# Kernel tuning notes

Hardware: AMD Instinct MI355X
Metric: run time of the kernel (lower is better)

## Reference

```python
import jax, jax.numpy as jnp
import numpy as np

D_INPUT = 900; D_MODEL = 900; D_STATE = 16; D_CONV = 4
D_INNER = 1800; DT_RANK = 57  # ceil(900/16)
B_SZ = 2; L = 900


def build_pe():
    # Faithful to the (non-standard) loop in PositionalEncoding.__init__
    pos = np.arange(D_INPUT, dtype=np.float64)[:, None]
    pe = np.zeros((D_INPUT, D_MODEL), dtype=np.float64)
    i_even = np.arange(0, D_MODEL, 2, dtype=np.float64)
    i_odd = np.arange(1, D_MODEL, 2, dtype=np.float64)
    pe[:, 0::2] = np.sin(pos / 10000.0 ** (2.0 * i_even / D_MODEL))
    pe[:, 1::2] = np.cos(pos / 10000.0 ** (2.0 * (i_odd + 1.0) / D_MODEL))
    return jnp.asarray(pe, jnp.float32)


def setup_inputs() -> dict:
    key = jax.random.key(0)
    ks = jax.random.split(key, 8)
    s = 0.02
    inp = jax.random.normal(ks[0], (B_SZ, L, D_INPUT), jnp.float32)
    W_emb = jax.random.normal(ks[1], (D_MODEL, D_INPUT), jnp.float32) * s
    b_emb = jnp.zeros((D_MODEL,), jnp.float32)
    norm_w = jnp.ones((D_MODEL,), jnp.float32)
    W_in = jax.random.normal(ks[2], (2 * D_INNER, D_MODEL), jnp.float32) * s
    conv_w = jax.random.normal(ks[3], (D_INNER, 1, D_CONV), jnp.float32) * s
    conv_b = jnp.zeros((D_INNER,), jnp.float32)
    W_xp = jax.random.normal(ks[4], (DT_RANK + 2 * D_STATE, D_INNER), jnp.float32) * s
    W_dt = jax.random.normal(ks[5], (D_INNER, DT_RANK), jnp.float32) * s
    b_dt = jnp.zeros((D_INNER,), jnp.float32)
    A_log = jnp.log(jnp.broadcast_to(jnp.arange(1, D_STATE + 1, dtype=jnp.float32), (D_INNER, D_STATE)))
    D = jnp.ones((D_INNER,), jnp.float32)
    W_out = jax.random.normal(ks[6], (D_MODEL, D_INNER), jnp.float32) * s
    normf_w = jnp.ones((D_MODEL,), jnp.float32)
    pe = build_pe()
    return dict(inp=inp, W_emb=W_emb, b_emb=b_emb, norm_w=norm_w, W_in=W_in,
                conv_w=conv_w, conv_b=conv_b, W_xp=W_xp, W_dt=W_dt, b_dt=b_dt,
                A_log=A_log, D=D, W_out=W_out, normf_w=normf_w, pe=pe)


def rmsnorm(x, w, eps=1e-5):
    return x * jax.lax.rsqrt(jnp.mean(x * x, axis=-1, keepdims=True) + eps) * w


def causal_dwconv(x, w, b):
    # x: (b, l, d_in); torch Conv1d(groups=d_in, padding=k-1) then [:, :, :l] == causal left-pad
    xc = jnp.transpose(x, (0, 2, 1))  # (b, d_in, l)
    y = jax.lax.conv_general_dilated(xc, w, window_strides=(1,),
                                     padding=[(D_CONV - 1, 0)],
                                     dimension_numbers=('NCH', 'OIH', 'NCH'),
                                     feature_group_count=D_INNER)
    return jnp.transpose(y + b[None, :, None], (0, 2, 1))


def selective_scan(u, delta, A, Bm, Cm, Dv):
    # u, delta: (b, l, d_in); A: (d_in, n); Bm, Cm: (b, l, n); Dv: (d_in,)
    dA = jnp.exp(jnp.einsum('bld,dn->bldn', delta, A))
    dBu = jnp.einsum('bld,bln,bld->bldn', delta, Bm, u)

    def step(h, xs):
        dA_i, dBu_i, C_i = xs
        h = dA_i * h + dBu_i                      # (b, d_in, n)
        y = jnp.einsum('bdn,bn->bd', h, C_i)
        return h, y

    h0 = jnp.zeros((u.shape[0], D_INNER, D_STATE), u.dtype)
    _, ys = jax.lax.scan(step, h0, (jnp.moveaxis(dA, 1, 0), jnp.moveaxis(dBu, 1, 0), jnp.moveaxis(Cm, 1, 0)))
    return jnp.moveaxis(ys, 0, 1) + u * Dv


def mamba_block(x, W_in, conv_w, conv_b, W_xp, W_dt, b_dt, A_log, Dv, W_out):
    xr = x @ W_in.T                               # (b, l, 2*d_inner)
    xm, res = xr[..., :D_INNER], xr[..., D_INNER:]
    xb = xm[..., ::-1]  # NOTE: original flips dim 2 == channel dim, not sequence
    xm = jax.nn.silu(causal_dwconv(xm, conv_w, conv_b))
    xb = jax.nn.silu(causal_dwconv(xb, conv_w, conv_b))

    def ssm(u):
        A = -jnp.exp(A_log)
        xd = u @ W_xp.T                           # (b, l, dt_rank + 2n)
        delta = jax.nn.softplus(xd[..., :DT_RANK] @ W_dt.T + b_dt)
        Bm = xd[..., DT_RANK:DT_RANK + D_STATE]
        Cm = xd[..., DT_RANK + D_STATE:]
        return selective_scan(u, delta, A, Bm, Cm, Dv)

    y = ssm(xm)
    yb = ssm(xb)[..., ::-1]  # flip back over channels, as in original
    g = jax.nn.silu(res)
    return (y * g + yb * g) @ W_out.T


def reference(inp, W_emb, b_emb, norm_w, W_in, conv_w, conv_b, W_xp, W_dt, b_dt, A_log, D, W_out, normf_w, pe):
    x = inp @ W_emb.T + b_emb                     # embedding Linear
    x = x * jnp.sqrt(jnp.float32(D_MODEL)) + pe[None, :x.shape[1]]
    x = mamba_block(rmsnorm(x, norm_w), W_in, conv_w, conv_b, W_xp, W_dt, b_dt, A_log, D, W_out) + x
    x = rmsnorm(x, normf_w)
    logits = x.reshape(x.shape[0], -1)
    return (logits,)
```

## Files before the change

### kernel.cpp

```cpp
#include <hip/hip_runtime.h>
#include <math.h>

typedef unsigned short ushortT;
typedef short short8 __attribute__((ext_vector_type(8)));
typedef float f32x4 __attribute__((ext_vector_type(4)));

#define D_STATE 16
#define D_INNER 1800
#define DT_RANK 57
#define SEQ_L 900
#define MROWS 1800
#define MP 1920
#define KP_DM 960
#define KP_DI 1856
#define KP_DT 64
#define NCHUNK 45
#define CLEN 20

__device__ __forceinline__ ushortT f2bf(float f) {
    unsigned u = __float_as_uint(f);
    unsigned r = (u + 0x7FFFu + ((u >> 16) & 1u)) >> 16;
    return (ushortT)r;
}
__device__ __forceinline__ float bf2f(ushortT h) {
    return __uint_as_float((unsigned)h << 16);
}
__device__ __forceinline__ float silu_f(float x) { return x / (1.f + __expf(-x)); }
__device__ __forceinline__ float softplus_f(float x) {
    return fmaxf(x, 0.f) + __logf(1.f + __expf(-fabsf(x)));
}

__device__ __forceinline__ void gload_lds16(const ushortT* g, ushortT* l) {
    __builtin_amdgcn_global_load_lds((const __attribute__((address_space(1))) unsigned int*)g,
                                     (__attribute__((address_space(3))) unsigned int*)l,
                                     16, 0, 0);
}

__global__ __launch_bounds__(256)
void cvt_all_k(const float* __restrict__ s0, ushortT* __restrict__ d0,
               const float* __restrict__ s1, ushortT* __restrict__ d1,
               const float* __restrict__ s2, ushortT* __restrict__ d2,
               const float* __restrict__ s3, ushortT* __restrict__ d3,
               const float* __restrict__ s4, ushortT* __restrict__ d4,
               const float* __restrict__ s5, ushortT* __restrict__ d5)
{
    const float* src; ushortT* dst; int M, K, Mp, Kp;
    switch (blockIdx.y) {
      case 0: src=s0; dst=d0; M=1800; K=900;  Mp=1920; Kp=960;  break;
      case 1: src=s1; dst=d1; M=900;  K=900;  Mp=1024; Kp=960;  break;
      case 2: src=s2; dst=d2; M=3600; K=900;  Mp=3712; Kp=960;  break;
      case 3: src=s3; dst=d3; M=89;   K=1800; Mp=128;  Kp=1856; break;
      case 4: src=s4; dst=d4; M=1800; K=57;   Mp=1920; Kp=64;   break;
      default:src=s5; dst=d5; M=900;  K=1800; Mp=1024; Kp=1856; break;
    }
    int t = blockIdx.x * 256 + threadIdx.x;
    int K4 = Kp >> 2;
    if (t >= Mp * K4) return;
    int r = t / K4, c4 = (t - r * K4) * 4;
    ushortT o[4];
#pragma unroll
    for (int e = 0; e < 4; ++e) {
        int c = c4 + e;
        float v = (r < M && c < K) ? src[(size_t)r * K + c] : 0.f;
        o[e] = f2bf(v);
    }
    uint2 pk;
    pk.x = (unsigned)o[0] | ((unsigned)o[1] << 16);
    pk.y = (unsigned)o[2] | ((unsigned)o[3] << 16);
    *(uint2*)(dst + (size_t)r * Kp + c4) = pk;
}

__global__ __launch_bounds__(256)
void gemm_mfma_k(const ushortT* __restrict__ A0, const ushortT* __restrict__ A1, int lda,
                 const ushortT* __restrict__ Bw, int ldb, int nkTotal, int split,
                 float* __restrict__ C0, float* __restrict__ C1, int ldc, size_t cstride,
                 ushortT* __restrict__ X0, ushortT* __restrict__ X1, int ldx, size_t xstride,
                 int M, int N, const float* __restrict__ bias, int mode)
{
    __shared__ ushortT As[128 * 64];
    __shared__ ushortT Bs[128 * 64];
    int z = blockIdx.z;
    int dir = z / split, s = z % split;
    int per = (nkTotal + split - 1) / split;
    int kt0 = s * per;
    int kcnt = nkTotal - kt0; if (kcnt > per) kcnt = per;

    const ushortT* A = dir ? A1 : A0;
    float* C = (dir ? C1 : C0);
    ushortT* Xo = (dir ? X1 : X0);
    if (C)  C  += (size_t)s * cstride;
    if (Xo) Xo += (size_t)s * xstride;

    int tid = threadIdx.x;
    int lane = tid & 63, wave = tid >> 6;
    int wr = wave >> 1, wc = wave & 1;
    int m0 = blockIdx.y * 128, n0 = blockIdx.x * 128;

    f32x4 acc[4][4] = {};

    for (int kt = kt0; kt < kt0 + kcnt; ++kt) {
#pragma unroll
        for (int r = 0; r < 4; ++r) {
            int idx = r * 256 + tid;
            int row = idx >> 3, c8 = (idx & 7) << 3;
            gload_lds16(A + (size_t)(m0 + row) * lda + kt * 64 + c8, As + idx * 8);
        }
#pragma unroll
        for (int r = 0; r < 4; ++r) {
            int idx = r * 256 + tid;
            int row = idx >> 3, c8 = (idx & 7) << 3;
            gload_lds16(Bw + (size_t)(n0 + row) * ldb + kt * 64 + c8, Bs + idx * 8);
        }
        __syncthreads();
#pragma unroll
        for (int ks = 0; ks < 2; ++ks) {
            short8 av[4], bv[4];
            int kcol = ks * 32 + (lane >> 4) * 8;
#pragma unroll
            for (int i = 0; i < 4; ++i)
                av[i] = *(const short8*)(As + (wr * 64 + i * 16 + (lane & 15)) * 64 + kcol);
#pragma unroll
            for (int j = 0; j < 4; ++j)
                bv[j] = *(const short8*)(Bs + (wc * 64 + j * 16 + (lane & 15)) * 64 + kcol);
#pragma unroll
            for (int i = 0; i < 4; ++i)
#pragma unroll
                for (int j = 0; j < 4; ++j)
                    acc[i][j] = __builtin_amdgcn_mfma_f32_16x16x32_bf16(bv[j], av[i], acc[i][j], 0, 0, 0);
        }
        __syncthreads();
    }

#pragma unroll
    for (int i = 0; i < 4; ++i) {
        int m = m0 + wr * 64 + i * 16 + (lane & 15);
        if (m >= M) continue;
#pragma unroll
        for (int j = 0; j < 4; ++j) {
            int nb = n0 + wc * 64 + j * 16 + (lane >> 4) * 4;
            if (nb >= N) continue;
            f32x4 v = acc[i][j];
            if (mode == 5) {
#pragma unroll
                for (int e = 0; e < 4; ++e)
                    v[e] = softplus_f(v[e] + bias[nb + e]);
            }
            if (mode == 1 || mode == 5) {
                unsigned lo, hi;
                asm("v_cvt_pk_bf16_f32 %0, %1, %2" : "=v"(lo) : "v"(v[0]), "v"(v[1]));
                asm("v_cvt_pk_bf16_f32 %0, %1, %2" : "=v"(hi) : "v"(v[2]), "v"(v[3]));
                uint2 pk; pk.x = lo; pk.y = hi;
                *(uint2*)(Xo + (size_t)m * ldx + nb) = pk;
            } else {
                *(f32x4*)(C + (size_t)m * ldc + nb) = v;
            }
        }
    }
}

__global__ __launch_bounds__(256)
void rmsnorm_emb_k(const ushortT* __restrict__ P, size_t pstride,
                   const float* __restrict__ b_emb, const float* __restrict__ pe,
                   const float* __restrict__ norm_w,
                   float* __restrict__ XS, ushortT* __restrict__ XN, int ldxn)
{
    int row = blockIdx.x;
    int l = (row >= SEQ_L) ? row - SEQ_L : row;
    float vv[4];
    float ssum = 0.f;
#pragma unroll
    for (int k = 0; k < 4; ++k) {
        int c = threadIdx.x + k * 256;
        if (c < 900) {
            size_t i = (size_t)row * 900 + c;
            float a = bf2f(P[i]) + bf2f(P[i + pstride]) + bf2f(P[i + 2 * pstride]) + bf2f(P[i + 3 * pstride]);
            float v = 30.f * (a + b_emb[c]) + pe[(size_t)l * 900 + c];
            vv[k] = v;
            ssum += v * v;
        } else vv[k] = 0.f;
    }
#pragma unroll
    for (int off = 32; off; off >>= 1) ssum += __shfl_down(ssum, off, 64);
    __shared__ float red[4];
    int wv = threadIdx.x >> 6;
    if ((threadIdx.x & 63) == 0) red[wv] = ssum;
    __syncthreads();
    float tot = red[0] + red[1] + red[2] + red[3];
    float scale = rsqrtf(tot / 900.f + 1e-5f);
#pragma unroll
    for (int k = 0; k < 4; ++k) {
        int c = threadIdx.x + k * 256;
        if (c < 900) {
            XS[(size_t)row * 900 + c] = vv[k];
            XN[(size_t)row * ldxn + c] = f2bf(vv[k] * scale * norm_w[c]);
        }
    }
}

__global__ __launch_bounds__(256)
void rmsnorm_final_k(const ushortT* __restrict__ ZP, size_t zstride,
                     const float* __restrict__ XS, const float* __restrict__ w,
                     float* __restrict__ out)
{
    int row = blockIdx.x;
    float vv[4];
    float ssum = 0.f;
#pragma unroll
    for (int k = 0; k < 4; ++k) {
        int c = threadIdx.x + k * 256;
        if (c < 900) {
            size_t i = (size_t)row * 900 + c;
            float v = bf2f(ZP[i]) + bf2f(ZP[i + zstride]) + bf2f(ZP[i + 2 * zstride]) + bf2f(ZP[i + 3 * zstride]) + XS[i];
            vv[k] = v;
            ssum += v * v;
        } else vv[k] = 0.f;
    }
#pragma unroll
    for (int off = 32; off; off >>= 1) ssum += __shfl_down(ssum, off, 64);
    __shared__ float red[4];
    int wv = threadIdx.x >> 6;
    if ((threadIdx.x & 63) == 0) red[wv] = ssum;
    __syncthreads();
    float tot = red[0] + red[1] + red[2] + red[3];
    float scale = rsqrtf(tot / 900.f + 1e-5f);
#pragma unroll
    for (int k = 0; k < 4; ++k) {
        int c = threadIdx.x + k * 256;
        if (c < 900) out[(size_t)row * 900 + c] = vv[k] * scale * w[c];
    }
}

__global__ __launch_bounds__(256)
void conv_silu_k(const ushortT* __restrict__ xr0, const ushortT* __restrict__ xr1,
                 const float* __restrict__ w, const float* __restrict__ cb,
                 ushortT* __restrict__ xmc, ushortT* __restrict__ xbc,
                 ushortT* __restrict__ gout)
{
    int t = blockIdx.x * 256 + threadIdx.x;
    if (t >= MROWS * (D_INNER / 2)) return;
    int d0 = (t % (D_INNER / 2)) * 2;
    int row = t / (D_INNER / 2);
    int l = row % SEQ_L;
    float w0[4], w1[4];
#pragma unroll
    for (int k = 0; k < 4; ++k) { w0[k] = w[d0 * 4 + k]; w1[k] = w[d0 * 4 + 4 + k]; }
    int rdp = 1798 - d0;
    float sf0 = cb[d0], sf1 = cb[d0 + 1];
    float sb0 = sf0, sb1 = sf1;
#pragma unroll
    for (int k = 0; k < 4; ++k) {
        int ll = l - 3 + k;
        if (ll < 0) continue;
        size_t ro = (size_t)(row - l + ll) * 3600;
        unsigned f0 = *(const unsigned*)(xr0 + ro + d0);
        unsigned f1 = *(const unsigned*)(xr1 + ro + d0);
        float a0 = bf2f((ushortT)f0) + bf2f((ushortT)f1);
        float a1 = bf2f((ushortT)(f0 >> 16)) + bf2f((ushortT)(f1 >> 16));
        sf0 = fmaf(w0[k], a0, sf0);
        sf1 = fmaf(w1[k], a1, sf1);
        unsigned r0 = *(const unsigned*)(xr0 + ro + rdp);
        unsigned r1 = *(const unsigned*)(xr1 + ro + rdp);
        float b0 = bf2f((ushortT)(r0 >> 16)) + bf2f((ushortT)(r1 >> 16));
        float b1 = bf2f((ushortT)r0) + bf2f((ushortT)r1);
        sb0 = fmaf(w0[k], b0, sb0);
        sb1 = fmaf(w1[k], b1, sb1);
    }
    unsigned om = (unsigned)f2bf(silu_f(sf0)) | ((unsigned)f2bf(silu_f(sf1)) << 16);
    unsigned ob = (unsigned)f2bf(silu_f(sb0)) | ((unsigned)f2bf(silu_f(sb1)) << 16);
    *(unsigned*)(xmc + (size_t)row * KP_DI + d0) = om;
    *(unsigned*)(xbc + (size_t)row * KP_DI + d0) = ob;
    size_t rr = (size_t)row * 3600 + D_INNER + d0;
    unsigned g0 = *(const unsigned*)(xr0 + rr);
    unsigned g1 = *(const unsigned*)(xr1 + rr);
    float ga = silu_f(bf2f((ushortT)g0) + bf2f((ushortT)g1));
    float gb = silu_f(bf2f((ushortT)(g0 >> 16)) + bf2f((ushortT)(g1 >> 16)));
    *(unsigned*)(gout + (size_t)row * D_INNER + d0) = (unsigned)f2bf(ga) | ((unsigned)f2bf(gb) << 16);
}

__global__ __launch_bounds__(256)
void xp_reduce_k(const float* __restrict__ XPp, size_t pstride,
                 float* __restrict__ XDC, ushortT* __restrict__ XDMb, ushortT* __restrict__ XDBb)
{
    int t = blockIdx.x * 256 + threadIdx.x;
    if (t >= 2 * MROWS * 96) return;
    int dir = t / (MROWS * 96);
    int rem = t - dir * (MROWS * 96);
    int row = rem / 96, c = rem - row * 96;
    const float* basep = XPp + (size_t)dir * 8 * pstride + (size_t)row * 96 + c;
    float s = 0.f;
#pragma unroll
    for (int p = 0; p < 8; ++p) s += basep[p * pstride];
    ushortT* xdb = dir ? XDBb : XDMb;
    if (c < DT_RANK)           xdb[(size_t)row * KP_DT + c] = f2bf(s);
    else if (c < KP_DT)        xdb[(size_t)row * KP_DT + c] = 0;
    if (c >= DT_RANK && c < DT_RANK + 2 * D_STATE)
        XDC[((size_t)dir * MROWS + row) * 32 + (c - DT_RANK)] = s;
}

__global__ __launch_bounds__(256)
void scan_l1_k(const ushortT* __restrict__ DMb, const ushortT* __restrict__ DBb,
               const ushortT* __restrict__ Um, const ushortT* __restrict__ Ub,
               const float* __restrict__ XDC, const float* __restrict__ A_log,
               float* __restrict__ HL, float* __restrict__ SD)
{
    int d = blockIdx.x * 256 + threadIdx.x;
    if (d >= D_INNER) return;
    int c = blockIdx.y, zz = blockIdx.z;
    int b = zz >> 1, dir = zz & 1;
    const ushortT* DL = dir ? DBb : DMb;
    const ushortT* U = dir ? Ub : Um;
    const float* XD = XDC + (size_t)dir * MROWS * 32;
    float Aa[D_STATE];
#pragma unroll
    for (int n = 0; n < D_STATE; ++n) Aa[n] = -__expf(A_log[d * D_STATE + n]);
    float h[D_STATE] = {};
    float S = 0.f;
    int l0 = c * CLEN;
    for (int i = 0; i < CLEN; ++i) {
        size_t rowi = (size_t)b * SEQ_L + l0 + i;
        float delta = bf2f(DL[rowi * D_INNER + d]);
        float u = bf2f(U[rowi * KP_DI + d]);
        const float* bc = XD + rowi * 32;
        float du = delta * u;
        S += delta;
#pragma unroll
        for (int n = 0; n < D_STATE; ++n)
            h[n] = fmaf(__expf(delta * Aa[n]), h[n], du * bc[n]);
    }
    float* hp = HL + ((size_t)(zz * NCHUNK + c) * D_INNER + d) * D_STATE;
#pragma unroll
    for (int q = 0; q < 4; ++q)
        *(f32x4*)(hp + q * 4) = f32x4{h[q*4], h[q*4+1], h[q*4+2], h[q*4+3]};
    SD[(size_t)(zz * NCHUNK + c) * D_INNER + d] = S;
}

__global__ __launch_bounds__(256)
void scan_l2_k(float* __restrict__ HL, const float* __restrict__ SD,
               const float* __restrict__ A_log)
{
    int t = blockIdx.x * 256 + threadIdx.x;
    if (t >= 4 * D_INNER * D_STATE) return;
    int n = t & 15;
    int d = (t >> 4) % D_INNER;
    int zz = t / (D_INNER * D_STATE);
    float Aa = -__expf(A_log[d * D_STATE + n]);
    float h0 = 0.f;
    for (int c = 0; c < NCHUNK; ++c) {
        size_t ih = ((size_t)(zz * NCHUNK + c) * D_INNER + d) * D_STATE + n;
        float hl = HL[ih];
        float T = __expf(Aa * SD[(size_t)(zz * NCHUNK + c) * D_INNER + d]);
        HL[ih] = h0;
        h0 = fmaf(T, h0, hl);
    }
}

__global__ __launch_bounds__(256)
void scan3_gate_k(const ushortT* __restrict__ DMb, const ushortT* __restrict__ DBb,
                  const ushortT* __restrict__ Um, const ushortT* __restrict__ Ub,
                  const float* __restrict__ XDC, const float* __restrict__ A_log,
                  const float* __restrict__ Dv, const float* __restrict__ HL,
                  const ushortT* __restrict__ G, ushortT* __restrict__ YC)
{
    int d = blockIdx.x * 256 + threadIdx.x;
    if (d >= D_INNER) return;
    int c = blockIdx.y, b = blockIdx.z;
    int rd = D_INNER - 1 - d;
    float Aa0[D_STATE], Aa1[D_STATE], h0[D_STATE], h1[D_STATE];
#pragma unroll
    for (int n = 0; n < D_STATE; ++n) Aa0[n] = -__expf(A_log[d * D_STATE + n]);
#pragma unroll
    for (int n = 0; n < D_STATE; ++n) Aa1[n] = -__expf(A_log[rd * D_STATE + n]);
    const float* hp0 = HL + ((size_t)((b * 2) * NCHUNK + c) * D_INNER + d) * D_STATE;
    const float* hp1 = HL + ((size_t)((b * 2 + 1) * NCHUNK + c) * D_INNER + rd) * D_STATE;
#pragma unroll
    for (int q = 0; q < 4; ++q) {
        f32x4 t0 = *(const f32x4*)(hp0 + q * 4);
        f32x4 t1 = *(const f32x4*)(hp1 + q * 4);
        h0[q*4] = t0[0]; h0[q*4+1] = t0[1]; h0[q*4+2] = t0[2]; h0[q*4+3] = t0[3];
        h1[q*4] = t1[0]; h1[q*4+1] = t1[1]; h1[q*4+2] = t1[2]; h1[q*4+3] = t1[3];
    }
    float Dd0 = Dv[d], Dd1 = Dv[rd];
    const float* XD0 = XDC;
    const float* XD1 = XDC + (size_t)MROWS * 32;
    int l0 = c * CLEN;
    for (int i = 0; i < CLEN; ++i) {
        size_t rowi = (size_t)b * SEQ_L + l0 + i;
        float delta0 = bf2f(DMb[rowi * D_INNER + d]);
        float u0 = bf2f(Um[rowi * KP_DI + d]);
        const float* bc0 = XD0 + rowi * 32;
        float du0 = delta0 * u0;
        float acc0 = u0 * Dd0;
#pragma unroll
        for (int n = 0; n < D_STATE; ++n) {
            h0[n] = fmaf(__expf(delta0 * Aa0[n]), h0[n], du0 * bc0[n]);
            acc0 = fmaf(h0[n], bc0[D_STATE + n], acc0);
        }
        float delta1 = bf2f(DBb[rowi * D_INNER + rd]);
        float u1 = bf2f(Ub[rowi * KP_DI + rd]);
        const float* bc1 = XD1 + rowi * 32;
        float du1 = delta1 * u1;
        float acc1 = u1 * Dd1;
#pragma unroll
        for (int n = 0; n < D_STATE; ++n) {
            h1[n] = fmaf(__expf(delta1 * Aa1[n]), h1[n], du1 * bc1[n]);
            acc1 = fmaf(h1[n], bc1[D_STATE + n], acc1);
        }
        float g = bf2f(G[rowi * D_INNER + d]);
        YC[rowi * KP_DI + d] = f2bf((acc0 + acc1) * g);
    }
}

extern "C" void kernel_launch(void* const* d_in, const int* in_sizes, int n_in,
                              void* d_out, int out_size, void* d_ws, size_t ws_size,
                              hipStream_t stream)
{
    const float* inp    = (const float*)d_in[0];
    const float* W_emb  = (const float*)d_in[1];
    const float* b_emb  = (const float*)d_in[2];
    const float* norm_w = (const float*)d_in[3];
    const float* W_in   = (const float*)d_in[4];
    const float* conv_w = (const float*)d_in[5];
    const float* conv_b = (const float*)d_in[6];
    const float* W_xp   = (const float*)d_in[7];
    const float* W_dt   = (const float*)d_in[8];
    const float* b_dt   = (const float*)d_in[9];
    const float* A_log  = (const float*)d_in[10];
    const float* Dv     = (const float*)d_in[11];
    const float* W_out  = (const float*)d_in[12];
    const float* normf_w= (const float*)d_in[13];
    const float* pe     = (const float*)d_in[14];

    char* base = (char*)d_ws;
    size_t off = 0;
    auto alloc = [&](size_t bytes) { char* p = base + off; off += (bytes + 255) & ~(size_t)255; return p; };

    float*   XS      = (float*)alloc(6480000);
    char*    arena1  = alloc(22032000);
    float*   XPp     = (float*)arena1;
    float*   HL      = (float*)arena1;
    float*   SD      = (float*)(arena1 + 20736000);
    ushortT* inp_bf  = (ushortT*)alloc(3686400);
    ushortT* XN_bf   = (ushortT*)alloc(3686400);
    ushortT* Wemb_bf = (ushortT*)alloc(1966080);
    ushortT* Win_bf  = (ushortT*)alloc(7127040);
    ushortT* Wxp_bf  = (ushortT*)alloc(475136);
    ushortT* Wdt_bf  = (ushortT*)alloc(245760);
    ushortT* Wout_bf = (ushortT*)alloc(3801088);
    ushortT* XBC_bf  = (ushortT*)alloc(7127040);
    char*    arena2  = alloc(25920000);
    ushortT* Pemb    = (ushortT*)arena2;
    ushortT* XR0     = (ushortT*)arena2;
    ushortT* XR1     = XR0 + (size_t)MROWS * 3600;
    ushortT* DMb     = (ushortT*)arena2;
    ushortT* DBb     = DMb + (size_t)MROWS * D_INNER;
    ushortT* ZP      = (ushortT*)arena2;
    ushortT* G_bf    = (ushortT*)alloc(6480000);

    float*   XDC     = (float*)Wemb_bf;
    ushortT* XDM_bf  = (ushortT*)((char*)Wemb_bf + 460800);
    ushortT* XDB_bf  = (ushortT*)((char*)Wemb_bf + 706560);
    ushortT* XMC_bf  = Win_bf;
    ushortT* YC_bf   = inp_bf;

    dim3 blk(256);
    auto cdiv = [](int a, int b) { return (a + b - 1) / b; };
    const size_t PSTR  = 1620000;
    const size_t XPSTR = 172800;
    const size_t XRSTR = (size_t)MROWS * 3600;

    hipLaunchKernelGGL(cvt_all_k, dim3(3480, 6), blk, 0, stream,
                       inp, inp_bf, W_emb, Wemb_bf, W_in, Win_bf,
                       W_xp, Wxp_bf, W_dt, Wdt_bf, W_out, Wout_bf);
    hipLaunchKernelGGL(gemm_mfma_k, dim3(8, 15, 4), blk, 0, stream,
                       inp_bf, inp_bf, KP_DM, Wemb_bf, KP_DM, KP_DM/64, 4,
                       (float*)nullptr, (float*)nullptr, 0, (size_t)0,
                       Pemb, Pemb, 900, PSTR,
                       MROWS, 900, (const float*)nullptr, 1);
    hipLaunchKernelGGL(rmsnorm_emb_k, dim3(MROWS), blk, 0, stream,
                       Pemb, PSTR, b_emb, pe, norm_w, XS, XN_bf, KP_DM);
    hipLaunchKernelGGL(gemm_mfma_k, dim3(29, 15, 2), blk, 0, stream,
                       XN_bf, XN_bf, KP_DM, Win_bf, KP_DM, KP_DM/64, 2,
                       (float*)nullptr, (float*)nullptr, 0, (size_t)0,
                       XR0, XR0, 3600, XRSTR,
                       MROWS, 3600, (const float*)nullptr, 1);
    hipLaunchKernelGGL(conv_silu_k, dim3(cdiv(MROWS * (D_INNER/2), 256)), blk, 0, stream,
                       XR0, XR1, conv_w, conv_b, XMC_bf, XBC_bf, G_bf);
    hipLaunchKernelGGL(gemm_mfma_k, dim3(1, 15, 16), blk, 0, stream,
                       XMC_bf, XBC_bf, KP_DI, Wxp_bf, KP_DI, KP_DI/64, 8,
                       XPp, XPp + 8 * XPSTR, 96, XPSTR,
                       (ushortT*)nullptr, (ushortT*)nullptr, 0, (size_t)0,
                       MROWS, 96, (const float*)nullptr, 0);
    hipLaunchKernelGGL(xp_reduce_k, dim3(cdiv(2 * MROWS * 96, 256)), blk, 0, stream,
                       XPp, XPSTR, XDC, XDM_bf, XDB_bf);
    hipLaunchKernelGGL(gemm_mfma_k, dim3(15, 15, 2), blk, 0, stream,
                       XDM_bf, XDB_bf, KP_DT, Wdt_bf, KP_DT, 1, 1,
                       (float*)nullptr, (float*)nullptr, 0, (size_t)0,
                       DMb, DBb, D_INNER, (size_t)0,
                       MROWS, D_INNER, b_dt, 5);
    hipLaunchKernelGGL(scan_l1_k, dim3(cdiv(D_INNER, 256), NCHUNK, 4), blk, 0, stream,
                       DMb, DBb, XMC_bf, XBC_bf, XDC, A_log, HL, SD);
    hipLaunchKernelGGL(scan_l2_k, dim3(cdiv(4 * D_INNER * D_STATE, 256)), blk, 0, stream, HL, SD, A_log);
    hipLaunchKernelGGL(scan3_gate_k, dim3(cdiv(D_INNER, 256), NCHUNK, 2), blk, 0, stream,
                       DMb, DBb, XMC_bf, XBC_bf, XDC, A_log, Dv, HL, G_bf, YC_bf);
    hipLaunchKernelGGL(gemm_mfma_k, dim3(8, 15, 4), blk, 0, stream,
                       YC_bf, YC_bf, KP_DI, Wout_bf, KP_DI, KP_DI/64, 4,
                       (float*)nullptr, (float*)nullptr, 0, (size_t)0,
                       ZP, ZP, 900, PSTR,
                       MROWS, 900, (const float*)nullptr, 1);
    hipLaunchKernelGGL(rmsnorm_final_k, dim3(MROWS), blk, 0, stream,
                       ZP, PSTR, XS, normf_w, (float*)d_out);
}
```

Before: 299.9 us.

## Double-buffer GEMM LDS tiles and store chunk scan states in bf16

The MFMA GEMM now uses two LDS buffers per operand, so the next k-tile's global-to-LDS loads are issued before computing on the current tile. Explicit vmcnt waits and raw barriers replace the two __syncthreads per iteration. Separately, the per-chunk scan carry states (HL) are stored as bf16 instead of fp32, halving their write and read traffic across the three scan kernels. The bf16 states lose precision in the carried recurrence, and the doubled LDS use may lower occupancy.

```diff
diff --git a/kernel.cpp b/kernel.cpp
--- a/kernel.cpp
+++ b/kernel.cpp
@@ -77,13 +77,14 @@
                  ushortT* __restrict__ X0, ushortT* __restrict__ X1, int ldx, size_t xstride,
                  int M, int N, const float* __restrict__ bias, int mode)
 {
-    __shared__ ushortT As[128 * 64];
-    __shared__ ushortT Bs[128 * 64];
+    __shared__ ushortT As[2][128 * 64];
+    __shared__ ushortT Bs[2][128 * 64];
     int z = blockIdx.z;
     int dir = z / split, s = z % split;
     int per = (nkTotal + split - 1) / split;
     int kt0 = s * per;
     int kcnt = nkTotal - kt0; if (kcnt > per) kcnt = per;
+    int ktEnd = kt0 + kcnt;
 
     const ushortT* A = dir ? A1 : A0;
     float* C = (dir ? C1 : C0);
@@ -96,39 +97,53 @@
     int wr = wave >> 1, wc = wave & 1;
     int m0 = blockIdx.y * 128, n0 = blockIdx.x * 128;
 
-    f32x4 acc[4][4] = {};
-
-    for (int kt = kt0; kt < kt0 + kcnt; ++kt) {
+    auto stage = [&](int sb, int kt) {
 #pragma unroll
         for (int r = 0; r < 4; ++r) {
             int idx = r * 256 + tid;
             int row = idx >> 3, c8 = (idx & 7) << 3;
-            gload_lds16(A + (size_t)(m0 + row) * lda + kt * 64 + c8, As + idx * 8);
+            gload_lds16(A + (size_t)(m0 + row) * lda + kt * 64 + c8, &As[sb][idx * 8]);
         }
 #pragma unroll
         for (int r = 0; r < 4; ++r) {
             int idx = r * 256 + tid;
             int row = idx >> 3, c8 = (idx & 7) << 3;
-            gload_lds16(Bw + (size_t)(n0 + row) * ldb + kt * 64 + c8, Bs + idx * 8);
-        }
-        __syncthreads();
+            gload_lds16(Bw + (size_t)(n0 + row) * ldb + kt * 64 + c8, &Bs[sb][idx * 8]);
+        }
+    };
+
+    f32x4 acc[4][4] = {};
+
+    stage(0, kt0);
+    for (int t = kt0; t < ktEnd; ++t) {
+        int cur = (t - kt0) & 1;
+        if (t + 1 < ktEnd) {
+            stage(cur ^ 1, t + 1);
+            asm volatile("s_waitcnt vmcnt(8)" ::: "memory");
+        } else {
+            asm volatile("s_waitcnt vmcnt(0)" ::: "memory");
+        }
+        __builtin_amdgcn_s_barrier();
+        __builtin_amdgcn_sched_barrier(0);
 #pragma unroll
         for (int ks = 0; ks < 2; ++ks) {
             short8 av[4], bv[4];
             int kcol = ks * 32 + (lane >> 4) * 8;
 #pragma unroll
             for (int i = 0; i < 4; ++i)
-                av[i] = *(const short8*)(As + (wr * 64 + i * 16 + (lane & 15)) * 64 + kcol);
+                av[i] = *(const short8*)(&As[cur][(wr * 64 + i * 16 + (lane & 15)) * 64 + kcol]);
 #pragma unroll
             for (int j = 0; j < 4; ++j)
-                bv[j] = *(const short8*)(Bs + (wc * 64 + j * 16 + (lane & 15)) * 64 + kcol);
+                bv[j] = *(const short8*)(&Bs[cur][(wc * 64 + j * 16 + (lane & 15)) * 64 + kcol]);
 #pragma unroll
             for (int i = 0; i < 4; ++i)
 #pragma unroll
                 for (int j = 0; j < 4; ++j)
                     acc[i][j] = __builtin_amdgcn_mfma_f32_16x16x32_bf16(bv[j], av[i], acc[i][j], 0, 0, 0);
         }
-        __syncthreads();
+        __builtin_amdgcn_sched_barrier(0);
+        __builtin_amdgcn_s_barrier();
+        __builtin_amdgcn_sched_barrier(0);
     }
 
 #pragma unroll
@@ -301,7 +316,7 @@
 void scan_l1_k(const ushortT* __restrict__ DMb, const ushortT* __restrict__ DBb,
                const ushortT* __restrict__ Um, const ushortT* __restrict__ Ub,
                const float* __restrict__ XDC, const float* __restrict__ A_log,
-               float* __restrict__ HL, float* __restrict__ SD)
+               ushortT* __restrict__ HL, float* __restrict__ SD)
 {
     int d = blockIdx.x * 256 + threadIdx.x;
     if (d >= D_INNER) return;
@@ -327,15 +342,20 @@
         for (int n = 0; n < D_STATE; ++n)
             h[n] = fmaf(__expf(delta * Aa[n]), h[n], du * bc[n]);
     }
-    float* hp = HL + ((size_t)(zz * NCHUNK + c) * D_INNER + d) * D_STATE;
-#pragma unroll
-    for (int q = 0; q < 4; ++q)
-        *(f32x4*)(hp + q * 4) = f32x4{h[q*4], h[q*4+1], h[q*4+2], h[q*4+3]};
+    ushortT* hp = HL + ((size_t)(zz * NCHUNK + c) * D_INNER + d) * D_STATE;
+    unsigned pk[8];
+#pragma unroll
+    for (int q = 0; q < 8; ++q)
+        asm("v_cvt_pk_bf16_f32 %0, %1, %2" : "=v"(pk[q]) : "v"(h[2*q]), "v"(h[2*q+1]));
+    uint4 lo4; lo4.x = pk[0]; lo4.y = pk[1]; lo4.z = pk[2]; lo4.w = pk[3];
+    uint4 hi4; hi4.x = pk[4]; hi4.y = pk[5]; hi4.z = pk[6]; hi4.w = pk[7];
+    *(uint4*)(hp) = lo4;
+    *(uint4*)(hp + 8) = hi4;
     SD[(size_t)(zz * NCHUNK + c) * D_INNER + d] = S;
 }
 
 __global__ __launch_bounds__(256)
-void scan_l2_k(float* __restrict__ HL, const float* __restrict__ SD,
+void scan_l2_k(ushortT* __restrict__ HL, const float* __restrict__ SD,
                const float* __restrict__ A_log)
 {
     int t = blockIdx.x * 256 + threadIdx.x;
@@ -347,9 +367,9 @@
     float h0 = 0.f;
     for (int c = 0; c < NCHUNK; ++c) {
         size_t ih = ((size_t)(zz * NCHUNK + c) * D_INNER + d) * D_STATE + n;
-        float hl = HL[ih];
+        float hl = bf2f(HL[ih]);
         float T = __expf(Aa * SD[(size_t)(zz * NCHUNK + c) * D_INNER + d]);
-        HL[ih] = h0;
+        HL[ih] = f2bf(h0);
         h0 = fmaf(T, h0, hl);
     }
 }
@@ -358,7 +378,7 @@
 void scan3_gate_k(const ushortT* __restrict__ DMb, const ushortT* __restrict__ DBb,
                   const ushortT* __restrict__ Um, const ushortT* __restrict__ Ub,
                   const float* __restrict__ XDC, const float* __restrict__ A_log,
-                  const float* __restrict__ Dv, const float* __restrict__ HL,
+                  const float* __restrict__ Dv, const ushortT* __restrict__ HL,
                   const ushortT* __restrict__ G, ushortT* __restrict__ YC)
 {
     int d = blockIdx.x * 256 + threadIdx.x;
@@ -370,14 +390,25 @@
     for (int n = 0; n < D_STATE; ++n) Aa0[n] = -__expf(A_log[d * D_STATE + n]);
 #pragma unroll
     for (int n = 0; n < D_STATE; ++n) Aa1[n] = -__expf(A_log[rd * D_STATE + n]);
-    const float* hp0 = HL + ((size_t)((b * 2) * NCHUNK + c) * D_INNER + d) * D_STATE;
-    const float* hp1 = HL + ((size_t)((b * 2 + 1) * NCHUNK + c) * D_INNER + rd) * D_STATE;
-#pragma unroll
-    for (int q = 0; q < 4; ++q) {
-        f32x4 t0 = *(const f32x4*)(hp0 + q * 4);
-        f32x4 t1 = *(const f32x4*)(hp1 + q * 4);
-        h0[q*4] = t0[0]; h0[q*4+1] = t0[1]; h0[q*4+2] = t0[2]; h0[q*4+3] = t0[3];
-        h1[q*4] = t1[0]; h1[q*4+1] = t1[1]; h1[q*4+2] = t1[2]; h1[q*4+3] = t1[3];
+    const ushortT* hp0 = HL + ((size_t)((b * 2) * NCHUNK + c) * D_INNER + d) * D_STATE;
+    const ushortT* hp1 = HL + ((size_t)((b * 2 + 1) * NCHUNK + c) * D_INNER + rd) * D_STATE;
+    {
+        uint4 a0 = *(const uint4*)(hp0);
+        uint4 a1 = *(const uint4*)(hp0 + 8);
+        unsigned ww[8] = {a0.x, a0.y, a0.z, a0.w, a1.x, a1.y, a1.z, a1.w};
+#pragma unroll
+        for (int q = 0; q < 8; ++q) {
+            h0[2*q]   = bf2f((ushortT)ww[q]);
+            h0[2*q+1] = bf2f((ushortT)(ww[q] >> 16));
+        }
+        uint4 b0 = *(const uint4*)(hp1);
+        uint4 b1 = *(const uint4*)(hp1 + 8);
+        unsigned vv[8] = {b0.x, b0.y, b0.z, b0.w, b1.x, b1.y, b1.z, b1.w};
+#pragma unroll
+        for (int q = 0; q < 8; ++q) {
+            h1[2*q]   = bf2f((ushortT)vv[q]);
+            h1[2*q+1] = bf2f((ushortT)(vv[q] >> 16));
+        }
     }
     float Dd0 = Dv[d], Dd1 = Dv[rd];
     const float* XD0 = XDC;
@@ -437,8 +468,8 @@
     float*   XS      = (float*)alloc(6480000);
     char*    arena1  = alloc(22032000);
     float*   XPp     = (float*)arena1;
-    float*   HL      = (float*)arena1;
-    float*   SD      = (float*)(arena1 + 20736000);
+    ushortT* HL      = (ushortT*)arena1;
+    float*   SD      = (float*)(arena1 + 10368000);
     ushortT* inp_bf  = (ushortT*)alloc(3686400);
     ushortT* XN_bf   = (ushortT*)alloc(3686400);
     ushortT* Wemb_bf = (ushortT*)alloc(1966080);
```

Result: no change. 295.3 us (-1.5%).
